# Kernel optimization log

Measured on AMD Instinct MI355X. Metric: run time of the kernel, lower is better.

Reference implementation:

```python
import jax, jax.numpy as jnp
import numpy as np

WIDTH = 1.0  # radial_width
AMPLITUDE = (WIDTH ** 0.5) * 1.772637204826652  # ~sqrt(pi*width)
BN_EPS = 1e-3  # keras BatchNormalization default


def sine_pos_encoding(seq_len, hidden, dtype):
    # keras_nlp.layers.SinePositionEncoding, max_wavelength=10000
    position = jnp.arange(seq_len, dtype=dtype)
    min_freq = jnp.asarray(1.0 / 10000.0, dtype)
    timescales = min_freq ** (2 * (jnp.arange(hidden) // 2).astype(dtype) / hidden)
    angles = position[:, None] * timescales[None, :]  # [T, H]
    odd = (jnp.arange(hidden) % 2).astype(dtype)
    return jnp.sin(angles) * (1 - odd) + jnp.cos(angles) * odd


def setup_inputs() -> dict:
    key = jax.random.key(0)
    ks = jax.random.split(key, 4)
    B, T, C, F, K, L = 16, 4096, 8, 64, 11, 4096
    x = jax.random.normal(ks[0], (B, T, C), jnp.float32)
    conv_w = jax.random.normal(ks[1], (K, C, F), jnp.float32) * 0.1
    conv_b = jnp.zeros((F,), jnp.float32)
    gamma = jnp.ones((F,), jnp.float32)
    beta = jnp.zeros((F,), jnp.float32)
    mean = jnp.zeros((F,), jnp.float32)
    var = jnp.ones((F,), jnp.float32)
    # HeNormal init for dense
    dense_w = jax.random.normal(ks[2], (F, L), jnp.float32) * (2.0 / F) ** 0.5
    dense_b = jnp.zeros((L,), jnp.float32)
    return dict(x=x, conv_w=conv_w, conv_b=conv_b, gamma=gamma, beta=beta,
                mean=mean, var=var, dense_w=dense_w, dense_b=dense_b)


def reference(x, conv_w, conv_b, gamma, beta, mean, var, dense_w, dense_b):
    B, T, C = x.shape
    F = conv_w.shape[-1]
    L = dense_w.shape[-1]
    # Conv1D same padding -> [B, T, F]
    h = jax.lax.conv_general_dilated(x, conv_w, (1,), 'SAME',
                                     dimension_numbers=('NWC', 'WIO', 'NWC')) + conv_b
    # BatchNorm (inference form)
    h = (h - mean) / jnp.sqrt(var + BN_EPS) * gamma + beta
    # Softmax over time axis
    h = jax.nn.softmax(h, axis=1)
    # sine positional encoding added
    h = h + sine_pos_encoding(T, F, x.dtype)
    # Dense with sigmoid, rescale to [-1, 1]
    d = jax.nn.sigmoid(h @ dense_w + dense_b) * 2.0 - 1.0  # [B, T, L]
    # ReductionLayer: sum over time -> shift weights [B, L]
    shift = jnp.sum(d, axis=1)
    # ShiftingLayer: Gaussian RBF warp matrix then matmul
    idx_in = jnp.arange(1, T + 1, dtype=x.dtype)                       # [T]
    scale = jnp.asarray(T / L, x.dtype)
    idx_sh = (jnp.arange(1, L + 1, dtype=x.dtype) + shift) * scale     # [B, L]
    M = idx_in[None, None, :] - idx_sh[:, :, None]                     # [B, L, T]
    M = jnp.exp(-(M * M) / WIDTH) / AMPLITUDE
    return jnp.matmul(M, x)  # [B, L, C]
```

## Files before the change

### kernel.cpp

```cpp
#include <hip/hip_runtime.h>
#include <stdint.h>

#define BB 16
#define TT 4096
#define CC 8
#define FF 64
#define KW 11
#define LL 4096

#define L2E 1.442695040888963f

typedef __attribute__((ext_vector_type(8))) short short8;
typedef __attribute__((ext_vector_type(16))) float floatx16;

__device__ float e_buf[(size_t)BB * TT * FF];

__device__ __forceinline__ unsigned short f2b(float f) {
    union { float f; uint32_t i; } v; v.f = f;
    uint32_t x = v.i;
    return (unsigned short)((x + 0x7fffu + ((x >> 16) & 1u)) >> 16);
}
__device__ __forceinline__ float b2f(unsigned short u) {
    union { uint32_t i; float f; } v; v.i = ((uint32_t)u) << 16; return v.f;
}

__global__ __launch_bounds__(256) void k_split(
        const float* __restrict__ dw, unsigned short* __restrict__ Wt) {
    const int idx  = blockIdx.x * 256 + threadIdx.x;
    const int j    = idx & 7;
    const int ln   = (idx >> 3) & 31;
    const int half = (idx >> 8) & 1;
    const int kf   = (idx >> 9) & 3;
    const int lt   = idx >> 11;
    const int l = lt * 32 + ln;
    const int k = kf * 16 + half * 8 + j;
    const float v = dw[(size_t)k * LL + l];
    const unsigned short hi = f2b(v);
    const unsigned short lo = f2b(v - b2f(hi));
    Wt[idx] = hi;
    Wt[262144 + idx] = lo;
}

__global__ __launch_bounds__(256) void k_conv(
        const float* __restrict__ x, const float* __restrict__ cw,
        const float* __restrict__ cb, const float* __restrict__ gm,
        const float* __restrict__ bt, const float* __restrict__ mn,
        const float* __restrict__ vr, float* __restrict__ sumexp) {
    __shared__ __align__(16) float xsm[(64 + KW - 1) * CC];
    __shared__ float red[4 * FF];
    const int tid = threadIdx.x;
    const int b  = blockIdx.x / (TT / 64);
    const int t0 = (blockIdx.x % (TT / 64)) * 64;
    const int f = tid & 63, ts = tid >> 6;

    float wreg[KW * CC];
#pragma unroll
    for (int kc = 0; kc < KW * CC; ++kc) wreg[kc] = cw[kc * FF + f];

    for (int i = tid; i < (64 + KW - 1) * CC; i += 256) {
        int row = i >> 3, c = i & 7;
        int t = t0 - (KW / 2) + row;
        xsm[i] = (t >= 0 && t < TT) ? x[((size_t)b * TT + t) * CC + c] : 0.0f;
    }
    const float s  = gm[f] * rsqrtf(vr[f] + 1e-3f);
    const float bb = bt[f] + (cb[f] - mn[f]) * s;
    const float s2 = s * L2E, b2 = bb * L2E;
    __syncthreads();

    float* eb = e_buf + ((size_t)b * TT + t0) * FF + f;
    const float4* xv = (const float4*)xsm;
    float esum = 0.f;
#pragma unroll 2
    for (int i = 0; i < 16; ++i) {
        const int tt = ts + 4 * i;
        float acc = 0.f;
#pragma unroll
        for (int k = 0; k < KW; ++k) {
            const float4 xa = xv[(tt + k) * 2];
            const float4 xb = xv[(tt + k) * 2 + 1];
            acc = fmaf(xa.x, wreg[k * 8 + 0], acc);
            acc = fmaf(xa.y, wreg[k * 8 + 1], acc);
            acc = fmaf(xa.z, wreg[k * 8 + 2], acc);
            acc = fmaf(xa.w, wreg[k * 8 + 3], acc);
            acc = fmaf(xb.x, wreg[k * 8 + 4], acc);
            acc = fmaf(xb.y, wreg[k * 8 + 5], acc);
            acc = fmaf(xb.z, wreg[k * 8 + 6], acc);
            acc = fmaf(xb.w, wreg[k * 8 + 7], acc);
        }
        float e = __builtin_amdgcn_exp2f(fmaf(acc, s2, b2));
        eb[tt * FF] = e;
        esum += e;
    }
    red[ts * FF + f] = esum;
    __syncthreads();
    if (ts == 0) {
        float tot = red[f] + red[FF + f] + red[2 * FF + f] + red[3 * FF + f];
        atomicAdd(&sumexp[b * FF + f], tot);
    }
}

__global__ __launch_bounds__(512) void k_main(
        const float* __restrict__ gm,  const float* __restrict__ bt,
        const float* __restrict__ mn,  const float* __restrict__ vr,
        const unsigned short* __restrict__ Wt,
        const float* __restrict__ db,  const float* __restrict__ sumexp,
        float* __restrict__ shiftsum) {
    __shared__ __align__(16) unsigned short As[16384];

    const int tid = threadIdx.x;
    const int b  = blockIdx.y;
    const int t0 = blockIdx.x * 128;
    const int f = tid & 63, tq = tid >> 6;

    const float inv_se = 1.0f / sumexp[b * FF + f];
    const float tsf = exp2f(-0.20762050586796017f * (float)(f & ~1));
    const int kfh = ((f >> 4) << 1) | ((f >> 3) & 1);
    const int jj  = f & 7;
    const float ang0 = (float)(t0 + tq) * tsf;
    const float dA = 8.0f * tsf;
    float sv = sinf(ang0), cv = cosf(ang0);
    const float sd = sinf(dA), cd = cosf(dA);

    const float* eb = e_buf + ((size_t)b * TT + t0) * FF + f;
#pragma unroll 4
    for (int i = 0; i < 16; ++i) {
        const int tt = tq + 8 * i;
        float ev = eb[tt * FF];
        float p = (f & 1) ? cv : sv;
        float h = fmaf(ev, inv_se, p);
        const unsigned short hi = f2b(h);
        const unsigned short lo = f2b(h - b2f(hi));
        const int off = ((tt >> 5) * 8 + kfh) * 256 + (tt & 31) * 8 + jj;
        As[off] = hi;
        As[8192 + off] = lo;
        float ns = fmaf(sv, cd, cv * sd);
        float nc = fmaf(cv, cd, -(sv * sd));
        sv = ns; cv = nc;
    }
    __syncthreads();

    const int lane = tid & 63;
    const int wv   = tid >> 6;
    const int half = lane >> 5;
    const int ln31 = lane & 31;
    const int vbase = (half << 9) | (ln31 << 4);
    const char* Ab = (const char*)As;
    const char* Wb = (const char*)Wt;

#pragma unroll 1
    for (int i = 0; i < 16; ++i) {
        const int lt = (i + 2 * wv) & 15;
        const int ltile = lt * 8 + wv;
        const int lbase = ltile * 32;
        const char* wp = Wb + ((size_t)ltile << 12) + vbase;
        short8 Whi[4], Wlo[4];
#pragma unroll
        for (int kf = 0; kf < 4; ++kf) {
            Whi[kf] = *reinterpret_cast<const short8*>(wp + kf * 1024);
            Wlo[kf] = *reinterpret_cast<const short8*>(wp + 524288 + kf * 1024);
        }
        const float dbn = db[lbase + ln31] * (-L2E);

        float ss[4] = {0.f, 0.f, 0.f, 0.f};
#pragma unroll
        for (int nt = 0; nt < 4; ++nt) {
            floatx16 acc = {0.f, 0.f, 0.f, 0.f, 0.f, 0.f, 0.f, 0.f,
                            0.f, 0.f, 0.f, 0.f, 0.f, 0.f, 0.f, 0.f};
            __builtin_amdgcn_s_setprio(1);
#pragma unroll
            for (int kf = 0; kf < 4; ++kf) {
                const int ao = (nt * 8 + kf * 2) << 9;
                short8 Ahi = *reinterpret_cast<const short8*>(Ab + ao + vbase);
                short8 Alo = *reinterpret_cast<const short8*>(Ab + 16384 + ao + vbase);
                acc = __builtin_amdgcn_mfma_f32_32x32x16_bf16(Ahi, Whi[kf], acc, 0, 0, 0);
                acc = __builtin_amdgcn_mfma_f32_32x32x16_bf16(Alo, Whi[kf], acc, 0, 0, 0);
                acc = __builtin_amdgcn_mfma_f32_32x32x16_bf16(Ahi, Wlo[kf], acc, 0, 0, 0);
            }
            __builtin_amdgcn_s_setprio(0);
#pragma unroll
            for (int q = 0; q < 4; ++q) {
                float e0 = __builtin_amdgcn_exp2f(fmaf(acc[4 * q + 0], -L2E, dbn));
                float e1 = __builtin_amdgcn_exp2f(fmaf(acc[4 * q + 1], -L2E, dbn));
                float e2 = __builtin_amdgcn_exp2f(fmaf(acc[4 * q + 2], -L2E, dbn));
                float e3 = __builtin_amdgcn_exp2f(fmaf(acc[4 * q + 3], -L2E, dbn));
                float a0 = 1.f + e0, a1 = 1.f + e1, a2 = 1.f + e2, a3 = 1.f + e3;
                float p01 = a0 * a1, p23 = a2 * a3;
                float num = fmaf(a0 + a1, p23, (a2 + a3) * p01);
                ss[q] = fmaf(num, __builtin_amdgcn_rcpf(p01 * p23), ss[q]);
            }
        }
        float ssum = (ss[0] + ss[1]) + (ss[2] + ss[3]);
        ssum += __shfl_xor(ssum, 32);
        if (half == 0)
            atomicAdd(shiftsum + (size_t)b * LL + lbase + ln31, ssum);
    }
}

__global__ __launch_bounds__(256) void k_warp(
        const float* __restrict__ shiftsum, const float* __restrict__ x,
        float* __restrict__ out) {
    const int idx = blockIdx.x * 256 + threadIdx.x;
    const int l = idx & (LL - 1);
    const int b = idx >> 12;
    const float sh = fmaf(2.0f, shiftsum[idx], -(float)TT);
    const float scale = (float)TT / (float)LL;
    const float center = ((float)(l + 1) + sh) * scale;
    const float R = 7.0f;
    int tlo = (int)ceilf(center - 1.0f - R);
    int thi = (int)floorf(center - 1.0f + R);
    if (tlo < 0) tlo = 0;
    if (thi > TT - 1) thi = TT - 1;
    float acc[CC];
#pragma unroll
    for (int c = 0; c < CC; ++c) acc[c] = 0.f;
    const float inv_amp = (float)(1.0 / 1.772637204826652);
    for (int t = tlo; t <= thi; ++t) {
        float d = (float)(t + 1) - center;
        float w = __expf(-d * d) * inv_amp;
        const float4 x0 = *reinterpret_cast<const float4*>(x + ((size_t)b * TT + t) * CC);
        const float4 x1 = *reinterpret_cast<const float4*>(x + ((size_t)b * TT + t) * CC + 4);
        acc[0] = fmaf(w, x0.x, acc[0]);
        acc[1] = fmaf(w, x0.y, acc[1]);
        acc[2] = fmaf(w, x0.z, acc[2]);
        acc[3] = fmaf(w, x0.w, acc[3]);
        acc[4] = fmaf(w, x1.x, acc[4]);
        acc[5] = fmaf(w, x1.y, acc[5]);
        acc[6] = fmaf(w, x1.z, acc[6]);
        acc[7] = fmaf(w, x1.w, acc[7]);
    }
    float* o = out + (size_t)idx * CC;
    *reinterpret_cast<float4*>(o)     = make_float4(acc[0], acc[1], acc[2], acc[3]);
    *reinterpret_cast<float4*>(o + 4) = make_float4(acc[4], acc[5], acc[6], acc[7]);
}

extern "C" void kernel_launch(void* const* d_in, const int* in_sizes, int n_in,
                              void* d_out, int out_size, void* d_ws, size_t ws_size,
                              hipStream_t stream) {
    const float* x  = (const float*)d_in[0];
    const float* cw = (const float*)d_in[1];
    const float* cb = (const float*)d_in[2];
    const float* gm = (const float*)d_in[3];
    const float* bt = (const float*)d_in[4];
    const float* mn = (const float*)d_in[5];
    const float* vr = (const float*)d_in[6];
    const float* dw = (const float*)d_in[7];
    const float* db = (const float*)d_in[8];

    float* sumexp      = (float*)d_ws;
    float* shiftsum    = sumexp + BB * FF;
    unsigned short* Wt = (unsigned short*)(shiftsum + BB * LL);

    hipMemsetAsync(sumexp, 0, (size_t)(BB * FF + BB * LL) * sizeof(float), stream);

    k_split<<<(FF * LL) / 256, 256, 0, stream>>>(dw, Wt);
    k_conv<<<BB * (TT / 64), 256, 0, stream>>>(x, cw, cb, gm, bt, mn, vr, sumexp);
    k_main<<<dim3(TT / 128, BB), 512, 0, stream>>>(gm, bt, mn, vr,
                                                   Wt, db, sumexp, shiftsum);
    k_warp<<<(BB * LL) / 256, 256, 0, stream>>>(shiftsum, x, (float*)d_out);
}
```

Before: 206.3 us.

## Merge weight split into conv kernel, register-block conv, split MFMA accumulators

The separate bf16 hi/lo weight-split kernel becomes extra blocks of the conv kernel, removing one launch. Each conv thread now computes four consecutive time steps and reuses every shared-memory x row across them, so fewer LDS loads are needed per output. In the main kernel the nt loop is no longer unrolled and the MFMA chain is split across two independent accumulators that are combined in the epilogue. This shortens the dependent MFMA chain but adds register pressure.

```diff
diff --git a/kernel.cpp b/kernel.cpp
--- a/kernel.cpp
+++ b/kernel.cpp
@@ -9,6 +9,7 @@
 #define LL 4096
 
 #define L2E 1.442695040888963f
+#define NCONV (BB * (TT / 64))
 
 typedef __attribute__((ext_vector_type(8))) short short8;
 typedef __attribute__((ext_vector_type(16))) float floatx16;
@@ -24,28 +25,34 @@
     union { uint32_t i; float f; } v; v.i = ((uint32_t)u) << 16; return v.f;
 }
 
-__global__ __launch_bounds__(256) void k_split(
-        const float* __restrict__ dw, unsigned short* __restrict__ Wt) {
-    const int idx  = blockIdx.x * 256 + threadIdx.x;
-    const int j    = idx & 7;
-    const int ln   = (idx >> 3) & 31;
-    const int half = (idx >> 8) & 1;
-    const int kf   = (idx >> 9) & 3;
-    const int lt   = idx >> 11;
-    const int l = lt * 32 + ln;
-    const int k = kf * 16 + half * 8 + j;
-    const float v = dw[(size_t)k * LL + l];
-    const unsigned short hi = f2b(v);
-    const unsigned short lo = f2b(v - b2f(hi));
-    Wt[idx] = hi;
-    Wt[262144 + idx] = lo;
-}
-
-__global__ __launch_bounds__(256) void k_conv(
+#define DOT8(acc, ra, rb, wp) \
+    acc = fmaf(ra.x, (wp)[0], acc); acc = fmaf(ra.y, (wp)[1], acc); \
+    acc = fmaf(ra.z, (wp)[2], acc); acc = fmaf(ra.w, (wp)[3], acc); \
+    acc = fmaf(rb.x, (wp)[4], acc); acc = fmaf(rb.y, (wp)[5], acc); \
+    acc = fmaf(rb.z, (wp)[6], acc); acc = fmaf(rb.w, (wp)[7], acc);
+
+__global__ __launch_bounds__(256) void k_convsplit(
         const float* __restrict__ x, const float* __restrict__ cw,
         const float* __restrict__ cb, const float* __restrict__ gm,
         const float* __restrict__ bt, const float* __restrict__ mn,
-        const float* __restrict__ vr, float* __restrict__ sumexp) {
+        const float* __restrict__ vr, const float* __restrict__ dw,
+        unsigned short* __restrict__ Wt, float* __restrict__ sumexp) {
+    if (blockIdx.x >= NCONV) {
+        const int idx  = (blockIdx.x - NCONV) * 256 + threadIdx.x;
+        const int j    = idx & 7;
+        const int ln   = (idx >> 3) & 31;
+        const int half = (idx >> 8) & 1;
+        const int kf   = (idx >> 9) & 3;
+        const int lt   = idx >> 11;
+        const int l = lt * 32 + ln;
+        const int k = kf * 16 + half * 8 + j;
+        const float v = dw[(size_t)k * LL + l];
+        const unsigned short hi = f2b(v);
+        const unsigned short lo = f2b(v - b2f(hi));
+        Wt[idx] = hi;
+        Wt[262144 + idx] = lo;
+        return;
+    }
     __shared__ __align__(16) float xsm[(64 + KW - 1) * CC];
     __shared__ float red[4 * FF];
     const int tid = threadIdx.x;
@@ -70,26 +77,28 @@
     float* eb = e_buf + ((size_t)b * TT + t0) * FF + f;
     const float4* xv = (const float4*)xsm;
     float esum = 0.f;
-#pragma unroll 2
-    for (int i = 0; i < 16; ++i) {
-        const int tt = ts + 4 * i;
-        float acc = 0.f;
-#pragma unroll
-        for (int k = 0; k < KW; ++k) {
-            const float4 xa = xv[(tt + k) * 2];
-            const float4 xb = xv[(tt + k) * 2 + 1];
-            acc = fmaf(xa.x, wreg[k * 8 + 0], acc);
-            acc = fmaf(xa.y, wreg[k * 8 + 1], acc);
-            acc = fmaf(xa.z, wreg[k * 8 + 2], acc);
-            acc = fmaf(xa.w, wreg[k * 8 + 3], acc);
-            acc = fmaf(xb.x, wreg[k * 8 + 4], acc);
-            acc = fmaf(xb.y, wreg[k * 8 + 5], acc);
-            acc = fmaf(xb.z, wreg[k * 8 + 6], acc);
-            acc = fmaf(xb.w, wreg[k * 8 + 7], acc);
+#pragma unroll 1
+    for (int c = 0; c < 4; ++c) {
+        const int tb = c * 16 + ts * 4;
+        float a0 = 0.f, a1 = 0.f, a2 = 0.f, a3 = 0.f;
+#pragma unroll
+        for (int k = 0; k < KW + 3; ++k) {
+            const float4 ra = xv[(tb + k) * 2];
+            const float4 rb = xv[(tb + k) * 2 + 1];
+            if (k <= 10)           { DOT8(a0, ra, rb, wreg + k * 8); }
+            if (k >= 1 && k <= 11) { DOT8(a1, ra, rb, wreg + (k - 1) * 8); }
+            if (k >= 2 && k <= 12) { DOT8(a2, ra, rb, wreg + (k - 2) * 8); }
+            if (k >= 3)            { DOT8(a3, ra, rb, wreg + (k - 3) * 8); }
         }
-        float e = __builtin_amdgcn_exp2f(fmaf(acc, s2, b2));
-        eb[tt * FF] = e;
-        esum += e;
+        float e0 = __builtin_amdgcn_exp2f(fmaf(a0, s2, b2));
+        float e1 = __builtin_amdgcn_exp2f(fmaf(a1, s2, b2));
+        float e2 = __builtin_amdgcn_exp2f(fmaf(a2, s2, b2));
+        float e3 = __builtin_amdgcn_exp2f(fmaf(a3, s2, b2));
+        eb[(tb + 0) * FF] = e0;
+        eb[(tb + 1) * FF] = e1;
+        eb[(tb + 2) * FF] = e2;
+        eb[(tb + 3) * FF] = e3;
+        esum += (e0 + e1) + (e2 + e3);
     }
     red[ts * FF + f] = esum;
     __syncthreads();
@@ -100,8 +109,6 @@
 }
 
 __global__ __launch_bounds__(512) void k_main(
-        const float* __restrict__ gm,  const float* __restrict__ bt,
-        const float* __restrict__ mn,  const float* __restrict__ vr,
         const unsigned short* __restrict__ Wt,
         const float* __restrict__ db,  const float* __restrict__ sumexp,
         float* __restrict__ shiftsum) {
@@ -162,27 +169,46 @@
         const float dbn = db[lbase + ln31] * (-L2E);
 
         float ss[4] = {0.f, 0.f, 0.f, 0.f};
-#pragma unroll
+#pragma unroll 1
         for (int nt = 0; nt < 4; ++nt) {
-            floatx16 acc = {0.f, 0.f, 0.f, 0.f, 0.f, 0.f, 0.f, 0.f,
-                            0.f, 0.f, 0.f, 0.f, 0.f, 0.f, 0.f, 0.f};
+            const char* ap = Ab + (nt << 12) + vbase;
+            floatx16 acc1 = {0.f, 0.f, 0.f, 0.f, 0.f, 0.f, 0.f, 0.f,
+                             0.f, 0.f, 0.f, 0.f, 0.f, 0.f, 0.f, 0.f};
+            floatx16 acc2 = acc1;
             __builtin_amdgcn_s_setprio(1);
-#pragma unroll
-            for (int kf = 0; kf < 4; ++kf) {
-                const int ao = (nt * 8 + kf * 2) << 9;
-                short8 Ahi = *reinterpret_cast<const short8*>(Ab + ao + vbase);
-                short8 Alo = *reinterpret_cast<const short8*>(Ab + 16384 + ao + vbase);
-                acc = __builtin_amdgcn_mfma_f32_32x32x16_bf16(Ahi, Whi[kf], acc, 0, 0, 0);
-                acc = __builtin_amdgcn_mfma_f32_32x32x16_bf16(Alo, Whi[kf], acc, 0, 0, 0);
-                acc = __builtin_amdgcn_mfma_f32_32x32x16_bf16(Ahi, Wlo[kf], acc, 0, 0, 0);
+            {
+                short8 Ahi = *reinterpret_cast<const short8*>(ap);
+                short8 Alo = *reinterpret_cast<const short8*>(ap + 16384);
+                acc1 = __builtin_amdgcn_mfma_f32_32x32x16_bf16(Ahi, Whi[0], acc1, 0, 0, 0);
+                acc1 = __builtin_amdgcn_mfma_f32_32x32x16_bf16(Alo, Whi[0], acc1, 0, 0, 0);
+                acc1 = __builtin_amdgcn_mfma_f32_32x32x16_bf16(Ahi, Wlo[0], acc1, 0, 0, 0);
+                Ahi = *reinterpret_cast<const short8*>(ap + 2048);
+                Alo = *reinterpret_cast<const short8*>(ap + 16384 + 2048);
+                acc2 = __builtin_amdgcn_mfma_f32_32x32x16_bf16(Ahi, Whi[2], acc2, 0, 0, 0);
+                acc2 = __builtin_amdgcn_mfma_f32_32x32x16_bf16(Alo, Whi[2], acc2, 0, 0, 0);
+                acc2 = __builtin_amdgcn_mfma_f32_32x32x16_bf16(Ahi, Wlo[2], acc2, 0, 0, 0);
+                Ahi = *reinterpret_cast<const short8*>(ap + 1024);
+                Alo = *reinterpret_cast<const short8*>(ap + 16384 + 1024);
+                acc1 = __builtin_amdgcn_mfma_f32_32x32x16_bf16(Ahi, Whi[1], acc1, 0, 0, 0);
+                acc1 = __builtin_amdgcn_mfma_f32_32x32x16_bf16(Alo, Whi[1], acc1, 0, 0, 0);
+                acc1 = __builtin_amdgcn_mfma_f32_32x32x16_bf16(Ahi, Wlo[1], acc1, 0, 0, 0);
+                Ahi = *reinterpret_cast<const short8*>(ap + 3072);
+                Alo = *reinterpret_cast<const short8*>(ap + 16384 + 3072);
+                acc2 = __builtin_amdgcn_mfma_f32_32x32x16_bf16(Ahi, Whi[3], acc2, 0, 0, 0);
+                acc2 = __builtin_amdgcn_mfma_f32_32x32x16_bf16(Alo, Whi[3], acc2, 0, 0, 0);
+                acc2 = __builtin_amdgcn_mfma_f32_32x32x16_bf16(Ahi, Wlo[3], acc2, 0, 0, 0);
             }
             __builtin_amdgcn_s_setprio(0);
 #pragma unroll
             for (int q = 0; q < 4; ++q) {
-                float e0 = __builtin_amdgcn_exp2f(fmaf(acc[4 * q + 0], -L2E, dbn));
-                float e1 = __builtin_amdgcn_exp2f(fmaf(acc[4 * q + 1], -L2E, dbn));
-                float e2 = __builtin_amdgcn_exp2f(fmaf(acc[4 * q + 2], -L2E, dbn));
-                float e3 = __builtin_amdgcn_exp2f(fmaf(acc[4 * q + 3], -L2E, dbn));
+                float e0 = __builtin_amdgcn_exp2f(fmaf(acc1[4 * q + 0], -L2E,
+                                                  fmaf(acc2[4 * q + 0], -L2E, dbn)));
+                float e1 = __builtin_amdgcn_exp2f(fmaf(acc1[4 * q + 1], -L2E,
+                                                  fmaf(acc2[4 * q + 1], -L2E, dbn)));
+                float e2 = __builtin_amdgcn_exp2f(fmaf(acc1[4 * q + 2], -L2E,
+                                                  fmaf(acc2[4 * q + 2], -L2E, dbn)));
+                float e3 = __builtin_amdgcn_exp2f(fmaf(acc1[4 * q + 3], -L2E,
+                                                  fmaf(acc2[4 * q + 3], -L2E, dbn)));
                 float a0 = 1.f + e0, a1 = 1.f + e1, a2 = 1.f + e2, a3 = 1.f + e3;
                 float p01 = a0 * a1, p23 = a2 * a3;
                 float num = fmaf(a0 + a1, p23, (a2 + a3) * p01);
@@ -252,9 +278,8 @@
 
     hipMemsetAsync(sumexp, 0, (size_t)(BB * FF + BB * LL) * sizeof(float), stream);
 
-    k_split<<<(FF * LL) / 256, 256, 0, stream>>>(dw, Wt);
-    k_conv<<<BB * (TT / 64), 256, 0, stream>>>(x, cw, cb, gm, bt, mn, vr, sumexp);
-    k_main<<<dim3(TT / 128, BB), 512, 0, stream>>>(gm, bt, mn, vr,
-                                                   Wt, db, sumexp, shiftsum);
+    k_convsplit<<<NCONV + (FF * LL) / 256, 256, 0, stream>>>(
+        x, cw, cb, gm, bt, mn, vr, dw, Wt, sumexp);
+    k_main<<<dim3(TT / 128, BB), 512, 0, stream>>>(Wt, db, sumexp, shiftsum);
     k_warp<<<(BB * LL) / 256, 256, 0, stream>>>(shiftsum, x, (float*)d_out);
 }
```

New measurement: 210.4 us. About the same (+2.0%).
